# Kernel tuning notes

Measured on AMD Instinct MI355X. Metric: run time of the kernel, lower is better.

Reference implementation:

```python
import jax, jax.numpy as jnp
import numpy as np

N = 100_000      # nodes
E = 1_600_000    # edges (avg degree 16)
IN_DIM = 256
HID = 128
N_OUT = 2


def _linear_params(key, fan_in, fan_out):
    kw, kb = jax.random.split(key)
    bound = 1.0 / np.sqrt(fan_in)
    W = jax.random.uniform(kw, (fan_in, fan_out), jnp.float32, -bound, bound)
    b = jax.random.uniform(kb, (fan_out,), jnp.float32, -bound, bound)
    return W, b


def setup_inputs() -> dict:
    key = jax.random.key(0)
    ks = jax.random.split(key, 6)
    edge_index = jax.random.randint(ks[0], (2, E), 0, N, dtype=jnp.int64)
    x = jax.random.normal(ks[1], (N, IN_DIM), jnp.float32)
    Wi, bi = _linear_params(ks[2], IN_DIM, HID)   # NodeInitializer.lin
    W1, b1 = _linear_params(ks[3], HID, HID)      # GCNConv 1
    W2, b2 = _linear_params(ks[4], HID, HID)      # GCNConv 2
    Wh, bh = _linear_params(ks[5], HID, N_OUT)    # head
    return {"edge_index": edge_index, "x": x, "Wi": Wi, "bi": bi,
            "W1": W1, "b1": b1, "W2": W2, "b2": b2, "Wh": Wh, "bh": bh}


def reference(edge_index, x, Wi, bi, W1, b1, W2, b2, Wh, bh):
    n = x.shape[0]
    # GCNConv preprocessing: add self-loops, symmetric degree normalization.
    loops = jnp.arange(n, dtype=edge_index.dtype)
    src = jnp.concatenate([edge_index[0], loops])  # message source
    dst = jnp.concatenate([edge_index[1], loops])  # aggregation target
    deg = jax.ops.segment_sum(jnp.ones(src.shape[0], jnp.float32), dst, num_segments=n)
    dinv = jnp.where(deg > 0, deg ** -0.5, 0.0)
    norm = dinv[src] * dinv[dst]                   # [E+N]

    # NodeInitializer: relu(linear(x)); dropout = identity (eval mode)
    h = jax.nn.relu(x @ Wi + bi)

    # Two GCNConv layers (no relu between, matching SimpleGCN.forward)
    for W, b in ((W1, b1), (W2, b2)):
        msg = (h @ W)[src] * norm[:, None]         # gather + normalize, [E+N, HID]
        h = jax.ops.segment_sum(msg, dst, num_segments=n) + b  # scatter-add

    return h @ Wh + bh                             # [N, N_OUT]
```

## Files before the change

kernel.cpp:

```cpp
#include <hip/hip_runtime.h>
#include <hip/hip_bf16.h>

#define N_NODES 100000
#define N_EDGES 1600000
#define DIM_IN  256
#define DIM_H   128

#define NBKT 782
#define CPAD 16
#define EPB  8192
#define NBLK ((N_EDGES + EPB - 1) / EPB)

typedef __attribute__((ext_vector_type(8))) short short8;
typedef __attribute__((ext_vector_type(4))) float f32x4;

__device__ __forceinline__ int get_src(const int* e, int is64, int i) {
  return is64 ? e[2 * i] : e[i];
}
__device__ __forceinline__ int get_dst(const int* e, int is64, int i) {
  return is64 ? e[2 * (N_EDGES + i)] : e[N_EDGES + i];
}

__global__ __launch_bounds__(1024)
void k_init(const int* __restrict__ e, int* __restrict__ flag,
            int* __restrict__ bcnt) {
  if (blockIdx.x == 0) {
    __shared__ int s;
    if (threadIdx.x == 0) s = 0;
    __syncthreads();
    atomicOr(&s, e[2 * threadIdx.x + 1]);
    __syncthreads();
    if (threadIdx.x == 0) *flag = (s == 0) ? 1 : 0;
  } else {
    int i = (blockIdx.x - 1) * 1024 + threadIdx.x;
    if (i < NBKT * CPAD) bcnt[i] = 0;
  }
}

__global__ __launch_bounds__(256) void k_zero(int* __restrict__ p, int n) {
  int i = blockIdx.x * 256 + threadIdx.x;
  if (i < n) p[i] = 0;
}

__global__ __launch_bounds__(1024)
void k_binc(const int* __restrict__ eidx, const int* __restrict__ flag,
            int* __restrict__ bcnt) {
  __shared__ int hist[NBKT];
  const int t = threadIdx.x;
  const int is64 = *flag;
  for (int i = t; i < NBKT; i += 1024) hist[i] = 0;
  __syncthreads();
#pragma unroll
  for (int j = 0; j < EPB / 1024; ++j) {
    int e = blockIdx.x * EPB + j * 1024 + t;
    if (e < N_EDGES) {
      unsigned s = (unsigned)get_src(eidx, is64, e);
      unsigned d = (unsigned)get_dst(eidx, is64, e);
      if (s < N_NODES && d < N_NODES) atomicAdd(&hist[d >> 7], 1);
    }
  }
  __syncthreads();
  for (int i = t; i < NBKT; i += 1024) {
    int h = hist[i];
    if (h) atomicAdd(&bcnt[i * CPAD], h);
  }
}

__global__ __launch_bounds__(1024)
void k_bscan(int* __restrict__ bcnt, int* __restrict__ bbase) {
  __shared__ int sm[1024];
  int t = threadIdx.x;
  int v = (t < NBKT) ? bcnt[t * CPAD] : 0;
  sm[t] = v;
  __syncthreads();
  for (int d = 1; d < 1024; d <<= 1) {
    int u = (t >= d) ? sm[t - d] : 0;
    __syncthreads();
    sm[t] += u;
    __syncthreads();
  }
  if (t < NBKT) {
    int excl = sm[t] - v;
    bbase[t] = excl;
    bcnt[t * CPAD] = excl;
    if (t == NBKT - 1) bbase[NBKT] = sm[t];
  }
}

__global__ __launch_bounds__(1024)
void k_bin(const int* __restrict__ eidx, const int* __restrict__ flag,
           int* __restrict__ bcnt, unsigned* __restrict__ ebuf) {
  __shared__ int hist[NBKT];
  __shared__ int cur[NBKT];
  const int t = threadIdx.x;
  const int is64 = *flag;
  for (int i = t; i < NBKT; i += 1024) hist[i] = 0;
  unsigned rec[EPB / 1024];
  int bkt[EPB / 1024];
  __syncthreads();
#pragma unroll
  for (int j = 0; j < EPB / 1024; ++j) {
    int e = blockIdx.x * EPB + j * 1024 + t;
    bkt[j] = -1;
    rec[j] = 0;
    if (e < N_EDGES) {
      unsigned s = (unsigned)get_src(eidx, is64, e);
      unsigned d = (unsigned)get_dst(eidx, is64, e);
      if (s < N_NODES && d < N_NODES) {
        bkt[j] = (int)(d >> 7);
        rec[j] = s | ((d & 127u) << 17);
        atomicAdd(&hist[bkt[j]], 1);
      }
    }
  }
  __syncthreads();
  for (int i = t; i < NBKT; i += 1024) {
    int h = hist[i];
    cur[i] = h ? atomicAdd(&bcnt[i * CPAD], h) : 0;
  }
  __syncthreads();
#pragma unroll
  for (int j = 0; j < EPB / 1024; ++j) {
    if (bkt[j] >= 0) {
      int pos = atomicAdd(&cur[bkt[j]], 1);
      ebuf[pos] = rec[j];
    }
  }
}

__global__ __launch_bounds__(256)
void k_csr(const int* __restrict__ bbase, const unsigned* __restrict__ ebuf,
           int* __restrict__ off, float* __restrict__ dinv,
           int* __restrict__ csr) {
  __shared__ int hist[128];
  __shared__ int scn[128];
  __shared__ int cur[128];
  const int b = blockIdx.x, t = threadIdx.x;
  const int n0 = b << 7;
  const int start = bbase[b], end = bbase[b + 1];
  if (t < 128) hist[t] = 0;
  __syncthreads();
  for (int i = start + t; i < end; i += 256) {
    atomicAdd(&hist[ebuf[i] >> 17], 1);
  }
  __syncthreads();
  if (t < 128) scn[t] = hist[t];
  __syncthreads();
  for (int d = 1; d < 128; d <<= 1) {
    int u = (t < 128 && t >= d) ? scn[t - d] : 0;
    __syncthreads();
    if (t < 128) scn[t] += u;
    __syncthreads();
  }
  if (t < 128) {
    int node = n0 + t;
    if (node < N_NODES) {
      off[node] = start + scn[t];
      dinv[node] = rsqrtf(1.0f + (float)hist[t]);
      cur[t] = start + scn[t] - hist[t];
    }
  }
  __syncthreads();
  for (int i = start + t; i < end; i += 256) {
    unsigned r = ebuf[i];
    int pos = atomicAdd(&cur[r >> 17], 1);
    csr[pos] = (int)(r & 0x1FFFFu);
  }
}

__device__ __forceinline__ ushort f2bf(float f) {
  unsigned u = __float_as_uint(f);
  unsigned r = (u + 0x7fffu + ((u >> 16) & 1u)) >> 16;
  return (ushort)r;
}
__device__ __forceinline__ float bf2f(ushort h) {
  return __uint_as_float(((unsigned)h) << 16);
}

__device__ __forceinline__ void load8(const float* p, float* o) {
  float4 a = reinterpret_cast<const float4*>(p)[0];
  float4 b = reinterpret_cast<const float4*>(p)[1];
  o[0] = a.x; o[1] = a.y; o[2] = a.z; o[3] = a.w;
  o[4] = b.x; o[5] = b.y; o[6] = b.z; o[7] = b.w;
}

__device__ __forceinline__ void cvt_split(const float* v, short8& h, short8& l) {
#pragma unroll
  for (int j = 0; j < 8; ++j) {
    ushort hb = f2bf(v[j]);
    ushort lb = f2bf(v[j] - bf2f(hb));
    h[j] = (short)hb;
    l[j] = (short)lb;
  }
}

__global__ __launch_bounds__(256)
void k_prep(const float* __restrict__ Wi, const float* __restrict__ W1,
            const float* __restrict__ W2, const float* __restrict__ Wh,
            const float* __restrict__ b1, const float* __restrict__ b2,
            const float* __restrict__ bh, ushort* __restrict__ outHi,
            float* __restrict__ Wcc) {
  __shared__ float Wc2s[DIM_H][2];
  constexpr int CH = DIM_IN / 32;
  if (blockIdx.x == 16) {
    const int t = threadIdx.x;
    const int i = t >> 1, j = t & 1;
    float s = 0.f;
#pragma unroll 4
    for (int m = 0; m < DIM_H; ++m) s += W2[(size_t)i * DIM_H + m] * Wh[m * 2 + j];
    Wc2s[i][j] = s;
    __syncthreads();
    float c = 0.f;
#pragma unroll 4
    for (int k = 0; k < DIM_H; ++k) c += W1[(size_t)i * DIM_H + k] * Wc2s[k][j];
    Wcc[i * 2 + j] = c;
    if (t < 2) {
      float a = 0.f, b = 0.f;
      for (int k = 0; k < DIM_H; ++k) {
        a += b1[k] * Wc2s[k][t];
        b += b2[k] * Wh[k * 2 + t];
      }
      Wcc[256 + t] = a;
      Wcc[258 + t] = b + bh[t];
    }
    return;
  }
  int idx = blockIdx.x * 256 + threadIdx.x;
  int n  = idx & 15;
  int qq = (idx >> 4) & 3;
  int nt = (idx >> 6) & 7;
  int c  = idx >> 9;
  int col = nt * 16 + n;
  short8 h8, l8;
#pragma unroll
  for (int j = 0; j < 8; ++j) {
    float v = Wi[(size_t)(c * 32 + qq * 8 + j) * DIM_H + col];
    ushort hb = f2bf(v);
    ushort lb = f2bf(v - bf2f(hb));
    h8[j] = (short)hb;
    l8[j] = (short)lb;
  }
  ((short8*)outHi)[idx] = h8;
  ((short8*)outHi)[CH * 512 + idx] = l8;
}

template <int K>
__global__ __launch_bounds__(256, 4)
void k_gemm_xz(const float* __restrict__ A, const ushort* __restrict__ Bfrag,
               const float* __restrict__ bias, const float* __restrict__ Wcc,
               const float* __restrict__ dinv, float4* __restrict__ tbl) {
  constexpr int CH = K / 32;
  __shared__ __align__(16) ushort AhiS[2][256 * 8];
  __shared__ __align__(16) ushort AloS[2][256 * 8];
  const int tid = threadIdx.x;
  const int m0 = blockIdx.x * 64;
  const int wave = tid >> 6, lane = tid & 63;
  const int m_l = lane & 15, quad = lane >> 4;
  const int rs = tid >> 2, q = tid & 3;

  f32x4 acc[2][4];
#pragma unroll
  for (int i = 0; i < 2; ++i)
#pragma unroll
    for (int j = 0; j < 4; ++j) acc[i][j] = (f32x4){0.f, 0.f, 0.f, 0.f};

  const short8* Bhi8 = (const short8*)Bfrag;
  const short8* Blo8 = Bhi8 + CH * 512;
  short8* Ah = (short8*)AhiS;
  short8* Al = (short8*)AloS;

  const int gr = m0 + rs;
  const float* Ap = &A[(size_t)((gr < N_NODES) ? gr : (N_NODES - 1)) * K + q * 8];
  const int went = (rs >> 4) * 64 + q * 16 + ((rs & 15) ^ (q << 2));
  const int rent = quad * 16 + (m_l ^ (quad << 2));

  {
    float v[8];
    load8(Ap, v);
    short8 h, l;
    cvt_split(v, h, l);
    Ah[went] = h;
    Al[went] = l;
  }
  const int bq = quad * 16 + m_l;
  short8 bh0 = Bhi8[(wave * 2 + 0) * 64 + bq];
  short8 bl0 = Blo8[(wave * 2 + 0) * 64 + bq];
  short8 bh1 = Bhi8[(wave * 2 + 1) * 64 + bq];
  short8 bl1 = Blo8[(wave * 2 + 1) * 64 + bq];
  __syncthreads();

#pragma unroll
  for (int c = 0; c < CH; ++c) {
    const int cur = c & 1, nxt = cur ^ 1;
    float vn[8];
    short8 nbh0, nbl0, nbh1, nbl1;
    if (c + 1 < CH) {
      load8(Ap + (c + 1) * 32, vn);
      const int b0 = ((c + 1) * 8 + wave * 2 + 0) * 64 + bq;
      const int b1 = ((c + 1) * 8 + wave * 2 + 1) * 64 + bq;
      nbh0 = Bhi8[b0]; nbl0 = Blo8[b0];
      nbh1 = Bhi8[b1]; nbl1 = Blo8[b1];
    }
    const short8* AhC = Ah + cur * 256;
    const short8* AlC = Al + cur * 256;
#pragma unroll
    for (int mt = 0; mt < 4; ++mt) {
      short8 ahi = AhC[mt * 64 + rent];
      short8 alo = AlC[mt * 64 + rent];
      acc[0][mt] = __builtin_amdgcn_mfma_f32_16x16x32_bf16(ahi, bh0, acc[0][mt], 0, 0, 0);
      acc[0][mt] = __builtin_amdgcn_mfma_f32_16x16x32_bf16(ahi, bl0, acc[0][mt], 0, 0, 0);
      acc[0][mt] = __builtin_amdgcn_mfma_f32_16x16x32_bf16(alo, bh0, acc[0][mt], 0, 0, 0);
      acc[1][mt] = __builtin_amdgcn_mfma_f32_16x16x32_bf16(ahi, bh1, acc[1][mt], 0, 0, 0);
      acc[1][mt] = __builtin_amdgcn_mfma_f32_16x16x32_bf16(ahi, bl1, acc[1][mt], 0, 0, 0);
      acc[1][mt] = __builtin_amdgcn_mfma_f32_16x16x32_bf16(alo, bh1, acc[1][mt], 0, 0, 0);
    }
    if (c + 1 < CH) {
      short8 h, l;
      cvt_split(vn, h, l);
      Ah[nxt * 256 + went] = h;
      Al[nxt * 256 + went] = l;
      bh0 = nbh0; bl0 = nbl0; bh1 = nbh1; bl1 = nbl1;
    }
    __syncthreads();
  }

  float p0[4][4], p1[4][4];
#pragma unroll
  for (int mt = 0; mt < 4; ++mt)
#pragma unroll
    for (int r = 0; r < 4; ++r) { p0[mt][r] = 0.f; p1[mt][r] = 0.f; }
#pragma unroll
  for (int ntl = 0; ntl < 2; ++ntl) {
    const int colg = (wave * 2 + ntl) * 16 + m_l;
    const float bv = bias[colg];
    const float w0 = Wcc[colg * 2 + 0];
    const float w1 = Wcc[colg * 2 + 1];
#pragma unroll
    for (int mt = 0; mt < 4; ++mt)
#pragma unroll
      for (int r = 0; r < 4; ++r) {
        float hv = fmaxf(acc[ntl][mt][r] + bv, 0.f);
        p0[mt][r] += hv * w0;
        p1[mt][r] += hv * w1;
      }
  }
#pragma unroll
  for (int o = 1; o < 16; o <<= 1) {
#pragma unroll
    for (int mt = 0; mt < 4; ++mt)
#pragma unroll
      for (int r = 0; r < 4; ++r) {
        p0[mt][r] += __shfl_xor(p0[mt][r], o);
        p1[mt][r] += __shfl_xor(p1[mt][r], o);
      }
  }
  float* zred = (float*)AhiS;
  if (m_l == 0) {
#pragma unroll
    for (int mt = 0; mt < 4; ++mt)
#pragma unroll
      for (int r = 0; r < 4; ++r) {
        zred[(((0 * 4 + wave) * 4 + quad) * 4 + mt) * 4 + r] = p0[mt][r];
        zred[(((1 * 4 + wave) * 4 + quad) * 4 + mt) * 4 + r] = p1[mt][r];
      }
  }
  __syncthreads();
  if (tid < 64) {
    const int mt = tid >> 4, qd = (tid >> 2) & 3, r = tid & 3;
    const int rowg = m0 + tid;
    if (rowg < N_NODES) {
      float s0 = 0.f, s1 = 0.f;
#pragma unroll
      for (int w = 0; w < 4; ++w) {
        s0 += zred[(((0 * 4 + w) * 4 + qd) * 4 + mt) * 4 + r];
        s1 += zred[(((1 * 4 + w) * 4 + qd) * 4 + mt) * 4 + r];
      }
      float dn = dinv[rowg];
      tbl[rowg] = make_float4(dn * s0, dn * s1, dn, 0.f);
    }
  }
}

__global__ __launch_bounds__(256)
void k_aggr1(const int* __restrict__ off, const int* __restrict__ csr,
             const float4* __restrict__ tbl, float2* __restrict__ tb2,
             float* __restrict__ g) {
  int node = blockIdx.x * 256 + threadIdx.x;
  if (node >= N_NODES) return;
  int start = (node == 0) ? 0 : off[node - 1];
  int end = off[node];
  float4 self = tbl[node];
  float s0 = self.x, s1 = self.y, sd = self.z;
  int e = start;
  for (; e + 3 < end; e += 4) {
    int i0 = csr[e], i1 = csr[e + 1], i2 = csr[e + 2], i3 = csr[e + 3];
    float4 v0 = tbl[i0];
    float4 v1 = tbl[i1];
    float4 v2 = tbl[i2];
    float4 v3 = tbl[i3];
    s0 += (v0.x + v1.x) + (v2.x + v3.x);
    s1 += (v0.y + v1.y) + (v2.y + v3.y);
    sd += (v0.z + v1.z) + (v2.z + v3.z);
  }
  for (; e < end; ++e) {
    float4 v = tbl[csr[e]];
    s0 += v.x; s1 += v.y; sd += v.z;
  }
  float dn = self.z;
  tb2[node] = make_float2(dn * dn * s0, dn * dn * s1);
  g[node] = dn * sd;
}

__global__ __launch_bounds__(256)
void k_aggr2(const int* __restrict__ off, const int* __restrict__ csr,
             const float2* __restrict__ tb2, const float* __restrict__ dinv,
             const float* __restrict__ g, const float* __restrict__ tail,
             float* __restrict__ out) {
  int node = blockIdx.x * 256 + threadIdx.x;
  if (node >= N_NODES) return;
  int start = (node == 0) ? 0 : off[node - 1];
  int end = off[node];
  float2 self = tb2[node];
  float s0 = self.x, s1 = self.y;
  int e = start;
  for (; e + 3 < end; e += 4) {
    int i0 = csr[e], i1 = csr[e + 1], i2 = csr[e + 2], i3 = csr[e + 3];
    float2 v0 = tb2[i0];
    float2 v1 = tb2[i1];
    float2 v2 = tb2[i2];
    float2 v3 = tb2[i3];
    s0 += (v0.x + v1.x) + (v2.x + v3.x);
    s1 += (v0.y + v1.y) + (v2.y + v3.y);
  }
  for (; e < end; ++e) {
    float2 v = tb2[csr[e]];
    s0 += v.x; s1 += v.y;
  }
  float dn = dinv[node], gv = g[node];
  float o0 = dn * s0 + gv * tail[0] + tail[2];
  float o1 = dn * s1 + gv * tail[1] + tail[3];
  reinterpret_cast<float2*>(out)[node] = make_float2(o0, o1);
}

__global__ __launch_bounds__(256) void k_count(const int* __restrict__ eidx,
                                               const int* __restrict__ flag,
                                               int* __restrict__ off) {
  int e = blockIdx.x * 256 + threadIdx.x;
  int is64 = *flag;
  if (e < N_EDGES) {
    unsigned d = (unsigned)get_dst(eidx, is64, e);
    if (d < N_NODES) atomicAdd(&off[d], 1);
  }
}

__global__ __launch_bounds__(256) void k_dinv_old(const int* __restrict__ off,
                                                  float* __restrict__ dinv) {
  int i = blockIdx.x * 256 + threadIdx.x;
  if (i < N_NODES) dinv[i] = rsqrtf(1.0f + (float)off[i]);
}

template <int K>
__global__ __launch_bounds__(256)
void k_gemm(const float* __restrict__ A, const float* __restrict__ B,
            const float* __restrict__ bias, const float* __restrict__ scale,
            float* __restrict__ C, const int do_relu) {
  __shared__ float As[64][33];
  const int tid = threadIdx.x;
  const int tx = tid & 15;
  const int ty = tid >> 4;
  const int m0 = blockIdx.x * 64;

  float acc[4][8];
#pragma unroll
  for (int i = 0; i < 4; ++i)
#pragma unroll
    for (int j = 0; j < 8; ++j) acc[i][j] = 0.f;

  const int rs = tid >> 2;
  const int ks = (tid & 3) * 8;

  for (int k0 = 0; k0 < K; k0 += 32) {
    float av8[8];
    const int gm = m0 + rs;
    if (gm < N_NODES) {
      load8(&A[(size_t)gm * K + k0 + ks], av8);
    } else {
#pragma unroll
      for (int j = 0; j < 8; ++j) av8[j] = 0.f;
    }
    __syncthreads();
#pragma unroll
    for (int j = 0; j < 8; ++j) As[rs][ks + j] = av8[j];
    __syncthreads();

    const float* Bp = B + (size_t)k0 * DIM_H + tx * 8;
#pragma unroll 4
    for (int k = 0; k < 32; ++k) {
      float bv[8];
      load8(Bp + (size_t)k * DIM_H, bv);
      float av[4];
#pragma unroll
      for (int rr = 0; rr < 4; ++rr) av[rr] = As[ty * 4 + rr][k];
#pragma unroll
      for (int rr = 0; rr < 4; ++rr)
#pragma unroll
        for (int cc = 0; cc < 8; ++cc)
          acc[rr][cc] = fmaf(av[rr], bv[cc], acc[rr][cc]);
    }
  }

  float bs[8];
  if (bias) {
    load8(bias + tx * 8, bs);
  } else {
#pragma unroll
    for (int j = 0; j < 8; ++j) bs[j] = 0.f;
  }
#pragma unroll
  for (int rr = 0; rr < 4; ++rr) {
    const int gm = m0 + ty * 4 + rr;
    if (gm < N_NODES) {
      float sc = scale ? scale[gm] : 1.0f;
      float v[8];
#pragma unroll
      for (int cc = 0; cc < 8; ++cc) {
        float t = acc[rr][cc] + bs[cc];
        if (do_relu) t = fmaxf(t, 0.f);
        v[cc] = t * sc;
      }
      float* Cp = &C[(size_t)gm * DIM_H + tx * 8];
      reinterpret_cast<float4*>(Cp)[0] = make_float4(v[0], v[1], v[2], v[3]);
      reinterpret_cast<float4*>(Cp)[1] = make_float4(v[4], v[5], v[6], v[7]);
    }
  }
}

__global__ __launch_bounds__(256)
void k_aggr_init(const float* __restrict__ t, const float* __restrict__ dinv,
                 const float* __restrict__ bias, float* __restrict__ h) {
  int idx = blockIdx.x * 256 + threadIdx.x;
  if (idx < N_NODES * DIM_H) {
    int i = idx >> 7;
    int c = idx & 127;
    float d = dinv[i];
    h[idx] = bias[c] + t[idx] * d * d;
  }
}

__global__ __launch_bounds__(256)
void k_aggr_edges(const int* __restrict__ eidx, const int* __restrict__ flag,
                  const float* __restrict__ t, const float* __restrict__ dinv,
                  float* __restrict__ h) {
  int e = blockIdx.x * 2 + (threadIdx.x >> 7);
  int c = threadIdx.x & 127;
  int is64 = *flag;
  if (e < N_EDGES) {
    unsigned s = (unsigned)get_src(eidx, is64, e);
    unsigned d = (unsigned)get_dst(eidx, is64, e);
    if (s < N_NODES && d < N_NODES) {
      float nrm = dinv[s] * dinv[d];
      unsafeAtomicAdd(&h[(size_t)d * DIM_H + c], t[(size_t)s * DIM_H + c] * nrm);
    }
  }
}

__global__ __launch_bounds__(256)
void k_head_f32(const float* __restrict__ h, const float* __restrict__ Wh,
                const float* __restrict__ bh, float* __restrict__ out) {
  int node = blockIdx.x * 4 + (threadIdx.x >> 6);
  int lane = threadIdx.x & 63;
  if (node >= N_NODES) return;
  float h0 = h[(size_t)node * DIM_H + lane];
  float h1 = h[(size_t)node * DIM_H + 64 + lane];
  float s0 = h0 * Wh[lane * 2 + 0] + h1 * Wh[(lane + 64) * 2 + 0];
  float s1 = h0 * Wh[lane * 2 + 1] + h1 * Wh[(lane + 64) * 2 + 1];
#pragma unroll
  for (int off = 32; off > 0; off >>= 1) {
    s0 += __shfl_down(s0, off);
    s1 += __shfl_down(s1, off);
  }
  if (lane == 0) {
    reinterpret_cast<float2*>(out)[node] = make_float2(s0 + bh[0], s1 + bh[1]);
  }
}

extern "C" void kernel_launch(void* const* d_in, const int* in_sizes, int n_in,
                              void* d_out, int out_size, void* d_ws, size_t ws_size,
                              hipStream_t stream) {
  (void)in_sizes; (void)n_in; (void)out_size;
  const int* eidx = (const int*)d_in[0];
  const float* x  = (const float*)d_in[1];
  const float* Wi = (const float*)d_in[2];
  const float* bi = (const float*)d_in[3];
  const float* W1 = (const float*)d_in[4];
  const float* b1 = (const float*)d_in[5];
  const float* W2 = (const float*)d_in[6];
  const float* b2 = (const float*)d_in[7];
  const float* Wh = (const float*)d_in[8];
  const float* bh = (const float*)d_in[9];
  float* out = (float*)d_out;

  const int gE  = (N_EDGES + 255) / 256;
  const int gM  = (N_NODES + 63) / 64;
  const int gW  = (N_NODES + 3) / 4;
  const int gN256 = (N_NODES + 255) / 256;

  char* ws = (char*)d_ws;
  int* flag = (int*)ws;

  const size_t need1 = 17410048;

  if (ws_size >= need1) {
    int*      bcnt  = (int*)(ws + 4096);
    int*      bbase = (int*)(ws + 57344);
    float*    Wcc   = (float*)(ws + 61440);
    ushort*   bfWi  = (ushort*)(ws + 65536);
    int*      off   = (int*)(ws + 262144);
    float*    dinv  = (float*)(ws + 720896);
    float*    g     = (float*)(ws + 1179648);
    float4*   tbl   = (float4*)(ws + 1638400);
    float2*   tb2   = (float2*)(ws + 3407872);
    int*      csr   = (int*)(ws + 4456448);
    unsigned* ebuf  = (unsigned*)(ws + 11010048);

    k_init<<<1 + (NBKT * CPAD + 1023) / 1024, 1024, 0, stream>>>(eidx, flag, bcnt);
    k_binc<<<NBLK, 1024, 0, stream>>>(eidx, flag, bcnt);
    k_bscan<<<1, 1024, 0, stream>>>(bcnt, bbase);
    k_bin<<<NBLK, 1024, 0, stream>>>(eidx, flag, bcnt, ebuf);
    k_csr<<<NBKT, 256, 0, stream>>>(bbase, ebuf, off, dinv, csr);

    k_prep<<<17, 256, 0, stream>>>(Wi, W1, W2, Wh, b1, b2, bh, bfWi, Wcc);

    k_gemm_xz<DIM_IN><<<gM, 256, 0, stream>>>(x, bfWi, bi, Wcc, dinv, tbl);
    k_aggr1<<<gN256, 256, 0, stream>>>(off, csr, tbl, tb2, g);
    k_aggr2<<<gN256, 256, 0, stream>>>(off, csr, tb2, dinv, g, Wcc + 256, out);
  } else {
    const int gN  = (N_NODES + 255) / 256;
    int*   off  = (int*)(ws + 4096);
    float* dinv = (float*)(ws + 404480);
    float* fbA  = (float*)(ws + 804864);
    float* fbB  = (float*)(ws + 804864 + (size_t)N_NODES * DIM_H * 4);
    const int gNH = (N_NODES * DIM_H + 255) / 256;
    const int gE2 = (N_EDGES + 1) / 2;
    k_init<<<1, 1024, 0, stream>>>(eidx, flag, (int*)(ws + 4096));
    k_zero<<<gN, 256, 0, stream>>>(off, N_NODES);
    k_count<<<gE, 256, 0, stream>>>(eidx, flag, off);
    k_dinv_old<<<gN, 256, 0, stream>>>(off, dinv);

    k_gemm<DIM_IN><<<gM, 256, 0, stream>>>(x, Wi, bi, nullptr, fbA, 1);
    k_gemm<DIM_H><<<gM, 256, 0, stream>>>(fbA, W1, nullptr, nullptr, fbB, 0);
    k_aggr_init<<<gNH, 256, 0, stream>>>(fbB, dinv, b1, fbA);
    k_aggr_edges<<<gE2, 256, 0, stream>>>(eidx, flag, fbB, dinv, fbA);
    k_gemm<DIM_H><<<gM, 256, 0, stream>>>(fbA, W2, nullptr, nullptr, fbB, 0);
    k_aggr_init<<<gNH, 256, 0, stream>>>(fbB, dinv, b2, fbA);
    k_aggr_edges<<<gE2, 256, 0, stream>>>(eidx, flag, fbB, dinv, fbA);
    k_head_f32<<<gW, 256, 0, stream>>>(fbA, Wh, bh, out);
  }
}
```

Before: 285.3 us.

## Replace CSR build and gather aggregation with atomic edge scatter

Drops the multi-kernel bucket sort and CSR construction (binc, bscan, bin, csr). Degrees are now counted with global atomics and the two aggregations become per-edge scatter kernels with float atomics into zeroed accumulators, each followed by a per-node finalize kernel. This removes the sorting passes and their large edge buffers, at the cost of contended global float atomics in every layer and non-deterministic summation order. The fallback path now also uses k_init to zero its buffers instead of k_zero.

```diff
diff --git a/kernel.cpp b/kernel.cpp
--- a/kernel.cpp
+++ b/kernel.cpp
@@ -6,24 +6,13 @@
 #define DIM_IN  256
 #define DIM_H   128
 
-#define NBKT 782
-#define CPAD 16
-#define EPB  8192
-#define NBLK ((N_EDGES + EPB - 1) / EPB)
-
 typedef __attribute__((ext_vector_type(8))) short short8;
 typedef __attribute__((ext_vector_type(4))) float f32x4;
 
-__device__ __forceinline__ int get_src(const int* e, int is64, int i) {
-  return is64 ? e[2 * i] : e[i];
-}
-__device__ __forceinline__ int get_dst(const int* e, int is64, int i) {
-  return is64 ? e[2 * (N_EDGES + i)] : e[N_EDGES + i];
-}
-
 __global__ __launch_bounds__(1024)
 void k_init(const int* __restrict__ e, int* __restrict__ flag,
-            int* __restrict__ bcnt) {
+            int* __restrict__ deg, float* __restrict__ z1,
+            float* __restrict__ z2) {
   if (blockIdx.x == 0) {
     __shared__ int s;
     if (threadIdx.x == 0) s = 0;
@@ -33,139 +22,27 @@
     if (threadIdx.x == 0) *flag = (s == 0) ? 1 : 0;
   } else {
     int i = (blockIdx.x - 1) * 1024 + threadIdx.x;
-    if (i < NBKT * CPAD) bcnt[i] = 0;
-  }
-}
-
-__global__ __launch_bounds__(256) void k_zero(int* __restrict__ p, int n) {
+    if (i < N_NODES) deg[i] = 0;
+    if (i < 4 * N_NODES) z1[i] = 0.f;
+    if (i < 2 * N_NODES) z2[i] = 0.f;
+  }
+}
+
+__global__ __launch_bounds__(256)
+void k_degc(const int* __restrict__ eidx, const int* __restrict__ flag,
+            int* __restrict__ deg) {
   int i = blockIdx.x * 256 + threadIdx.x;
-  if (i < n) p[i] = 0;
-}
-
-__global__ __launch_bounds__(1024)
-void k_binc(const int* __restrict__ eidx, const int* __restrict__ flag,
-            int* __restrict__ bcnt) {
-  __shared__ int hist[NBKT];
-  const int t = threadIdx.x;
+  if (i >= N_EDGES) return;
   const int is64 = *flag;
-  for (int i = t; i < NBKT; i += 1024) hist[i] = 0;
-  __syncthreads();
-#pragma unroll
-  for (int j = 0; j < EPB / 1024; ++j) {
-    int e = blockIdx.x * EPB + j * 1024 + t;
-    if (e < N_EDGES) {
-      unsigned s = (unsigned)get_src(eidx, is64, e);
-      unsigned d = (unsigned)get_dst(eidx, is64, e);
-      if (s < N_NODES && d < N_NODES) atomicAdd(&hist[d >> 7], 1);
-    }
-  }
-  __syncthreads();
-  for (int i = t; i < NBKT; i += 1024) {
-    int h = hist[i];
-    if (h) atomicAdd(&bcnt[i * CPAD], h);
-  }
-}
-
-__global__ __launch_bounds__(1024)
-void k_bscan(int* __restrict__ bcnt, int* __restrict__ bbase) {
-  __shared__ int sm[1024];
-  int t = threadIdx.x;
-  int v = (t < NBKT) ? bcnt[t * CPAD] : 0;
-  sm[t] = v;
-  __syncthreads();
-  for (int d = 1; d < 1024; d <<= 1) {
-    int u = (t >= d) ? sm[t - d] : 0;
-    __syncthreads();
-    sm[t] += u;
-    __syncthreads();
-  }
-  if (t < NBKT) {
-    int excl = sm[t] - v;
-    bbase[t] = excl;
-    bcnt[t * CPAD] = excl;
-    if (t == NBKT - 1) bbase[NBKT] = sm[t];
-  }
-}
-
-__global__ __launch_bounds__(1024)
-void k_bin(const int* __restrict__ eidx, const int* __restrict__ flag,
-           int* __restrict__ bcnt, unsigned* __restrict__ ebuf) {
-  __shared__ int hist[NBKT];
-  __shared__ int cur[NBKT];
-  const int t = threadIdx.x;
-  const int is64 = *flag;
-  for (int i = t; i < NBKT; i += 1024) hist[i] = 0;
-  unsigned rec[EPB / 1024];
-  int bkt[EPB / 1024];
-  __syncthreads();
-#pragma unroll
-  for (int j = 0; j < EPB / 1024; ++j) {
-    int e = blockIdx.x * EPB + j * 1024 + t;
-    bkt[j] = -1;
-    rec[j] = 0;
-    if (e < N_EDGES) {
-      unsigned s = (unsigned)get_src(eidx, is64, e);
-      unsigned d = (unsigned)get_dst(eidx, is64, e);
-      if (s < N_NODES && d < N_NODES) {
-        bkt[j] = (int)(d >> 7);
-        rec[j] = s | ((d & 127u) << 17);
-        atomicAdd(&hist[bkt[j]], 1);
-      }
-    }
-  }
-  __syncthreads();
-  for (int i = t; i < NBKT; i += 1024) {
-    int h = hist[i];
-    cur[i] = h ? atomicAdd(&bcnt[i * CPAD], h) : 0;
-  }
-  __syncthreads();
-#pragma unroll
-  for (int j = 0; j < EPB / 1024; ++j) {
-    if (bkt[j] >= 0) {
-      int pos = atomicAdd(&cur[bkt[j]], 1);
-      ebuf[pos] = rec[j];
-    }
-  }
-}
-
-__global__ __launch_bounds__(256)
-void k_csr(const int* __restrict__ bbase, const unsigned* __restrict__ ebuf,
-           int* __restrict__ off, float* __restrict__ dinv,
-           int* __restrict__ csr) {
-  __shared__ int hist[128];
-  __shared__ int scn[128];
-  __shared__ int cur[128];
-  const int b = blockIdx.x, t = threadIdx.x;
-  const int n0 = b << 7;
-  const int start = bbase[b], end = bbase[b + 1];
-  if (t < 128) hist[t] = 0;
-  __syncthreads();
-  for (int i = start + t; i < end; i += 256) {
-    atomicAdd(&hist[ebuf[i] >> 17], 1);
-  }
-  __syncthreads();
-  if (t < 128) scn[t] = hist[t];
-  __syncthreads();
-  for (int d = 1; d < 128; d <<= 1) {
-    int u = (t < 128 && t >= d) ? scn[t - d] : 0;
-    __syncthreads();
-    if (t < 128) scn[t] += u;
-    __syncthreads();
-  }
-  if (t < 128) {
-    int node = n0 + t;
-    if (node < N_NODES) {
-      off[node] = start + scn[t];
-      dinv[node] = rsqrtf(1.0f + (float)hist[t]);
-      cur[t] = start + scn[t] - hist[t];
-    }
-  }
-  __syncthreads();
-  for (int i = start + t; i < end; i += 256) {
-    unsigned r = ebuf[i];
-    int pos = atomicAdd(&cur[r >> 17], 1);
-    csr[pos] = (int)(r & 0x1FFFFu);
-  }
+  unsigned s, d;
+  if (is64) {
+    s = (unsigned)((const int2*)eidx)[i].x;
+    d = (unsigned)((const int2*)eidx)[N_EDGES + i].x;
+  } else {
+    s = (unsigned)eidx[i];
+    d = (unsigned)eidx[N_EDGES + i];
+  }
+  if (s < N_NODES && d < N_NODES) atomicAdd(&deg[d], 1);
 }
 
 __device__ __forceinline__ ushort f2bf(float f) {
@@ -248,7 +125,7 @@
 __global__ __launch_bounds__(256, 4)
 void k_gemm_xz(const float* __restrict__ A, const ushort* __restrict__ Bfrag,
                const float* __restrict__ bias, const float* __restrict__ Wcc,
-               const float* __restrict__ dinv, float4* __restrict__ tbl) {
+               const int* __restrict__ deg, float4* __restrict__ tbl) {
   constexpr int CH = K / 32;
   __shared__ __align__(16) ushort AhiS[2][256 * 8];
   __shared__ __align__(16) ushort AloS[2][256 * 8];
@@ -375,71 +252,82 @@
         s0 += zred[(((0 * 4 + w) * 4 + qd) * 4 + mt) * 4 + r];
         s1 += zred[(((1 * 4 + w) * 4 + qd) * 4 + mt) * 4 + r];
       }
-      float dn = dinv[rowg];
+      float dn = rsqrtf(1.0f + (float)deg[rowg]);
       tbl[rowg] = make_float4(dn * s0, dn * s1, dn, 0.f);
     }
   }
 }
 
 __global__ __launch_bounds__(256)
-void k_aggr1(const int* __restrict__ off, const int* __restrict__ csr,
-             const float4* __restrict__ tbl, float2* __restrict__ tb2,
-             float* __restrict__ g) {
-  int node = blockIdx.x * 256 + threadIdx.x;
-  if (node >= N_NODES) return;
-  int start = (node == 0) ? 0 : off[node - 1];
-  int end = off[node];
-  float4 self = tbl[node];
-  float s0 = self.x, s1 = self.y, sd = self.z;
-  int e = start;
-  for (; e + 3 < end; e += 4) {
-    int i0 = csr[e], i1 = csr[e + 1], i2 = csr[e + 2], i3 = csr[e + 3];
-    float4 v0 = tbl[i0];
-    float4 v1 = tbl[i1];
-    float4 v2 = tbl[i2];
-    float4 v3 = tbl[i3];
-    s0 += (v0.x + v1.x) + (v2.x + v3.x);
-    s1 += (v0.y + v1.y) + (v2.y + v3.y);
-    sd += (v0.z + v1.z) + (v2.z + v3.z);
-  }
-  for (; e < end; ++e) {
-    float4 v = tbl[csr[e]];
-    s0 += v.x; s1 += v.y; sd += v.z;
-  }
-  float dn = self.z;
-  tb2[node] = make_float2(dn * dn * s0, dn * dn * s1);
-  g[node] = dn * sd;
-}
-
-__global__ __launch_bounds__(256)
-void k_aggr2(const int* __restrict__ off, const int* __restrict__ csr,
-             const float2* __restrict__ tb2, const float* __restrict__ dinv,
-             const float* __restrict__ g, const float* __restrict__ tail,
-             float* __restrict__ out) {
-  int node = blockIdx.x * 256 + threadIdx.x;
-  if (node >= N_NODES) return;
-  int start = (node == 0) ? 0 : off[node - 1];
-  int end = off[node];
-  float2 self = tb2[node];
-  float s0 = self.x, s1 = self.y;
-  int e = start;
-  for (; e + 3 < end; e += 4) {
-    int i0 = csr[e], i1 = csr[e + 1], i2 = csr[e + 2], i3 = csr[e + 3];
-    float2 v0 = tb2[i0];
-    float2 v1 = tb2[i1];
-    float2 v2 = tb2[i2];
-    float2 v3 = tb2[i3];
-    s0 += (v0.x + v1.x) + (v2.x + v3.x);
-    s1 += (v0.y + v1.y) + (v2.y + v3.y);
-  }
-  for (; e < end; ++e) {
-    float2 v = tb2[csr[e]];
-    s0 += v.x; s1 += v.y;
-  }
-  float dn = dinv[node], gv = g[node];
-  float o0 = dn * s0 + gv * tail[0] + tail[2];
-  float o1 = dn * s1 + gv * tail[1] + tail[3];
-  reinterpret_cast<float2*>(out)[node] = make_float2(o0, o1);
+void k_scat1(const int* __restrict__ eidx, const int* __restrict__ flag,
+             const float4* __restrict__ tbl, float4* __restrict__ acc1) {
+  int i = blockIdx.x * 256 + threadIdx.x;
+  if (i >= N_EDGES) return;
+  const int is64 = *flag;
+  unsigned s, d;
+  if (is64) {
+    s = (unsigned)((const int2*)eidx)[i].x;
+    d = (unsigned)((const int2*)eidx)[N_EDGES + i].x;
+  } else {
+    s = (unsigned)eidx[i];
+    d = (unsigned)eidx[N_EDGES + i];
+  }
+  if (s < N_NODES && d < N_NODES) {
+    float4 t = tbl[s];
+    float* a = (float*)(acc1 + d);
+    unsafeAtomicAdd(a + 0, t.x);
+    unsafeAtomicAdd(a + 1, t.y);
+    unsafeAtomicAdd(a + 2, t.z);
+  }
+}
+
+__global__ __launch_bounds__(256)
+void k_fin1(const float4* __restrict__ acc1, const float4* __restrict__ tbl,
+            float2* __restrict__ tb2, float* __restrict__ g) {
+  int n = blockIdx.x * 256 + threadIdx.x;
+  if (n >= N_NODES) return;
+  float4 a = acc1[n];
+  float4 t = tbl[n];
+  float dn = t.z;
+  tb2[n] = make_float2(dn * dn * (a.x + t.x), dn * dn * (a.y + t.y));
+  g[n] = dn * (a.z + t.z);
+}
+
+__global__ __launch_bounds__(256)
+void k_scat2(const int* __restrict__ eidx, const int* __restrict__ flag,
+             const float2* __restrict__ tb2, float2* __restrict__ acc2) {
+  int i = blockIdx.x * 256 + threadIdx.x;
+  if (i >= N_EDGES) return;
+  const int is64 = *flag;
+  unsigned s, d;
+  if (is64) {
+    s = (unsigned)((const int2*)eidx)[i].x;
+    d = (unsigned)((const int2*)eidx)[N_EDGES + i].x;
+  } else {
+    s = (unsigned)eidx[i];
+    d = (unsigned)eidx[N_EDGES + i];
+  }
+  if (s < N_NODES && d < N_NODES) {
+    float2 t = tb2[s];
+    float* a = (float*)(acc2 + d);
+    unsafeAtomicAdd(a + 0, t.x);
+    unsafeAtomicAdd(a + 1, t.y);
+  }
+}
+
+__global__ __launch_bounds__(256)
+void k_fin2(const float2* __restrict__ acc2, const float2* __restrict__ tb2,
+            const float4* __restrict__ tbl, const float* __restrict__ g,
+            const float* __restrict__ tail, float* __restrict__ out) {
+  int n = blockIdx.x * 256 + threadIdx.x;
+  if (n >= N_NODES) return;
+  float2 a = acc2[n];
+  float2 y = tb2[n];
+  float dn = tbl[n].z;
+  float gv = g[n];
+  float o0 = dn * (y.x + a.x) + gv * tail[0] + tail[2];
+  float o1 = dn * (y.y + a.y) + gv * tail[1] + tail[3];
+  reinterpret_cast<float2*>(out)[n] = make_float2(o0, o1);
 }
 
 __global__ __launch_bounds__(256) void k_count(const int* __restrict__ eidx,
@@ -448,7 +336,8 @@
   int e = blockIdx.x * 256 + threadIdx.x;
   int is64 = *flag;
   if (e < N_EDGES) {
-    unsigned d = (unsigned)get_dst(eidx, is64, e);
+    unsigned d = is64 ? (unsigned)((const int2*)eidx)[N_EDGES + e].x
+                      : (unsigned)eidx[N_EDGES + e];
     if (d < N_NODES) atomicAdd(&off[d], 1);
   }
 }
@@ -555,8 +444,9 @@
   int c = threadIdx.x & 127;
   int is64 = *flag;
   if (e < N_EDGES) {
-    unsigned s = (unsigned)get_src(eidx, is64, e);
-    unsigned d = (unsigned)get_dst(eidx, is64, e);
+    unsigned s = is64 ? (unsigned)((const int2*)eidx)[e].x : (unsigned)eidx[e];
+    unsigned d = is64 ? (unsigned)((const int2*)eidx)[N_EDGES + e].x
+                      : (unsigned)eidx[N_EDGES + e];
     if (s < N_NODES && d < N_NODES) {
       float nrm = dinv[s] * dinv[d];
       unsafeAtomicAdd(&h[(size_t)d * DIM_H + c], t[(size_t)s * DIM_H + c] * nrm);
@@ -604,48 +494,44 @@
   const int gM  = (N_NODES + 63) / 64;
   const int gW  = (N_NODES + 3) / 4;
   const int gN256 = (N_NODES + 255) / 256;
+  const int gZ  = 1 + (4 * N_NODES + 1023) / 1024;
 
   char* ws = (char*)d_ws;
   int* flag = (int*)ws;
 
-  const size_t need1 = 17410048;
+  const size_t need1 = 5739264;
 
   if (ws_size >= need1) {
-    int*      bcnt  = (int*)(ws + 4096);
-    int*      bbase = (int*)(ws + 57344);
-    float*    Wcc   = (float*)(ws + 61440);
-    ushort*   bfWi  = (ushort*)(ws + 65536);
-    int*      off   = (int*)(ws + 262144);
-    float*    dinv  = (float*)(ws + 720896);
-    float*    g     = (float*)(ws + 1179648);
-    float4*   tbl   = (float4*)(ws + 1638400);
-    float2*   tb2   = (float2*)(ws + 3407872);
-    int*      csr   = (int*)(ws + 4456448);
-    unsigned* ebuf  = (unsigned*)(ws + 11010048);
-
-    k_init<<<1 + (NBKT * CPAD + 1023) / 1024, 1024, 0, stream>>>(eidx, flag, bcnt);
-    k_binc<<<NBLK, 1024, 0, stream>>>(eidx, flag, bcnt);
-    k_bscan<<<1, 1024, 0, stream>>>(bcnt, bbase);
-    k_bin<<<NBLK, 1024, 0, stream>>>(eidx, flag, bcnt, ebuf);
-    k_csr<<<NBKT, 256, 0, stream>>>(bbase, ebuf, off, dinv, csr);
+    float*  Wcc  = (float*)(ws + 4096);
+    ushort* bfWi = (ushort*)(ws + 8192);
+    int*    deg  = (int*)(ws + 139264);
+    float4* tbl  = (float4*)(ws + 539264);
+    float4* acc1 = (float4*)(ws + 2139264);
+    float2* tb2  = (float2*)(ws + 3739264);
+    float*  g    = (float*)(ws + 4539264);
+    float2* acc2 = (float2*)(ws + 4939264);
+
+    k_init<<<gZ, 1024, 0, stream>>>(eidx, flag, deg, (float*)acc1, (float*)acc2);
+    k_degc<<<gE, 256, 0, stream>>>(eidx, flag, deg);
 
     k_prep<<<17, 256, 0, stream>>>(Wi, W1, W2, Wh, b1, b2, bh, bfWi, Wcc);
 
-    k_gemm_xz<DIM_IN><<<gM, 256, 0, stream>>>(x, bfWi, bi, Wcc, dinv, tbl);
-    k_aggr1<<<gN256, 256, 0, stream>>>(off, csr, tbl, tb2, g);
-    k_aggr2<<<gN256, 256, 0, stream>>>(off, csr, tb2, dinv, g, Wcc + 256, out);
+    k_gemm_xz<DIM_IN><<<gM, 256, 0, stream>>>(x, bfWi, bi, Wcc, deg, tbl);
+
+    k_scat1<<<gE, 256, 0, stream>>>(eidx, flag, tbl, acc1);
+    k_fin1<<<gN256, 256, 0, stream>>>(acc1, tbl, tb2, g);
+    k_scat2<<<gE, 256, 0, stream>>>(eidx, flag, tb2, acc2);
+    k_fin2<<<gN256, 256, 0, stream>>>(acc2, tb2, tbl, g, Wcc + 256, out);
   } else {
-    const int gN  = (N_NODES + 255) / 256;
     int*   off  = (int*)(ws + 4096);
     float* dinv = (float*)(ws + 404480);
     float* fbA  = (float*)(ws + 804864);
     float* fbB  = (float*)(ws + 804864 + (size_t)N_NODES * DIM_H * 4);
     const int gNH = (N_NODES * DIM_H + 255) / 256;
     const int gE2 = (N_EDGES + 1) / 2;
-    k_init<<<1, 1024, 0, stream>>>(eidx, flag, (int*)(ws + 4096));
-    k_zero<<<gN, 256, 0, stream>>>(off, N_NODES);
+    k_init<<<gZ, 1024, 0, stream>>>(eidx, flag, off, fbA, fbB);
     k_count<<<gE, 256, 0, stream>>>(eidx, flag, off);
-    k_dinv_old<<<gN, 256, 0, stream>>>(off, dinv);
+    k_dinv_old<<<gN256, 256, 0, stream>>>(off, dinv);
 
     k_gemm<DIM_IN><<<gM, 256, 0, stream>>>(x, Wi, bi, nullptr, fbA, 1);
     k_gemm<DIM_H><<<gM, 256, 0, stream>>>(fbA, W1, nullptr, nullptr, fbB, 0);
```

After: 689.5 us. 2.42x slower.

## Replace full CSR build with fixed-capacity bucket lists and shared-memory aggregation

Applied to the files above, without the earlier changes.

Drops the count, scan, bin and CSR kernels. Edges are now binned in one pass into per-bucket slots of fixed capacity (CAP=4096 per 128-node bucket). Degrees and both aggregation passes work per bucket with shared-memory float atomics, instead of per-node CSR walks. The int64 detection is folded into the binning kernel and the counter zeroing into the prep kernel. This removes several launches and a full edge reorder pass. The risks are overflow if a bucket gets more than CAP edges, nondeterministic float summation order, and shared atomic contention.

```diff
diff --git a/kernel.cpp b/kernel.cpp
--- a/kernel.cpp
+++ b/kernel.cpp
@@ -8,6 +8,7 @@
 
 #define NBKT 782
 #define CPAD 16
+#define CAP  4096
 #define EPB  8192
 #define NBLK ((N_EDGES + EPB - 1) / EPB)
 
@@ -19,153 +20,6 @@
 }
 __device__ __forceinline__ int get_dst(const int* e, int is64, int i) {
   return is64 ? e[2 * (N_EDGES + i)] : e[N_EDGES + i];
-}
-
-__global__ __launch_bounds__(1024)
-void k_init(const int* __restrict__ e, int* __restrict__ flag,
-            int* __restrict__ bcnt) {
-  if (blockIdx.x == 0) {
-    __shared__ int s;
-    if (threadIdx.x == 0) s = 0;
-    __syncthreads();
-    atomicOr(&s, e[2 * threadIdx.x + 1]);
-    __syncthreads();
-    if (threadIdx.x == 0) *flag = (s == 0) ? 1 : 0;
-  } else {
-    int i = (blockIdx.x - 1) * 1024 + threadIdx.x;
-    if (i < NBKT * CPAD) bcnt[i] = 0;
-  }
-}
-
-__global__ __launch_bounds__(256) void k_zero(int* __restrict__ p, int n) {
-  int i = blockIdx.x * 256 + threadIdx.x;
-  if (i < n) p[i] = 0;
-}
-
-__global__ __launch_bounds__(1024)
-void k_binc(const int* __restrict__ eidx, const int* __restrict__ flag,
-            int* __restrict__ bcnt) {
-  __shared__ int hist[NBKT];
-  const int t = threadIdx.x;
-  const int is64 = *flag;
-  for (int i = t; i < NBKT; i += 1024) hist[i] = 0;
-  __syncthreads();
-#pragma unroll
-  for (int j = 0; j < EPB / 1024; ++j) {
-    int e = blockIdx.x * EPB + j * 1024 + t;
-    if (e < N_EDGES) {
-      unsigned s = (unsigned)get_src(eidx, is64, e);
-      unsigned d = (unsigned)get_dst(eidx, is64, e);
-      if (s < N_NODES && d < N_NODES) atomicAdd(&hist[d >> 7], 1);
-    }
-  }
-  __syncthreads();
-  for (int i = t; i < NBKT; i += 1024) {
-    int h = hist[i];
-    if (h) atomicAdd(&bcnt[i * CPAD], h);
-  }
-}
-
-__global__ __launch_bounds__(1024)
-void k_bscan(int* __restrict__ bcnt, int* __restrict__ bbase) {
-  __shared__ int sm[1024];
-  int t = threadIdx.x;
-  int v = (t < NBKT) ? bcnt[t * CPAD] : 0;
-  sm[t] = v;
-  __syncthreads();
-  for (int d = 1; d < 1024; d <<= 1) {
-    int u = (t >= d) ? sm[t - d] : 0;
-    __syncthreads();
-    sm[t] += u;
-    __syncthreads();
-  }
-  if (t < NBKT) {
-    int excl = sm[t] - v;
-    bbase[t] = excl;
-    bcnt[t * CPAD] = excl;
-    if (t == NBKT - 1) bbase[NBKT] = sm[t];
-  }
-}
-
-__global__ __launch_bounds__(1024)
-void k_bin(const int* __restrict__ eidx, const int* __restrict__ flag,
-           int* __restrict__ bcnt, unsigned* __restrict__ ebuf) {
-  __shared__ int hist[NBKT];
-  __shared__ int cur[NBKT];
-  const int t = threadIdx.x;
-  const int is64 = *flag;
-  for (int i = t; i < NBKT; i += 1024) hist[i] = 0;
-  unsigned rec[EPB / 1024];
-  int bkt[EPB / 1024];
-  __syncthreads();
-#pragma unroll
-  for (int j = 0; j < EPB / 1024; ++j) {
-    int e = blockIdx.x * EPB + j * 1024 + t;
-    bkt[j] = -1;
-    rec[j] = 0;
-    if (e < N_EDGES) {
-      unsigned s = (unsigned)get_src(eidx, is64, e);
-      unsigned d = (unsigned)get_dst(eidx, is64, e);
-      if (s < N_NODES && d < N_NODES) {
-        bkt[j] = (int)(d >> 7);
-        rec[j] = s | ((d & 127u) << 17);
-        atomicAdd(&hist[bkt[j]], 1);
-      }
-    }
-  }
-  __syncthreads();
-  for (int i = t; i < NBKT; i += 1024) {
-    int h = hist[i];
-    cur[i] = h ? atomicAdd(&bcnt[i * CPAD], h) : 0;
-  }
-  __syncthreads();
-#pragma unroll
-  for (int j = 0; j < EPB / 1024; ++j) {
-    if (bkt[j] >= 0) {
-      int pos = atomicAdd(&cur[bkt[j]], 1);
-      ebuf[pos] = rec[j];
-    }
-  }
-}
-
-__global__ __launch_bounds__(256)
-void k_csr(const int* __restrict__ bbase, const unsigned* __restrict__ ebuf,
-           int* __restrict__ off, float* __restrict__ dinv,
-           int* __restrict__ csr) {
-  __shared__ int hist[128];
-  __shared__ int scn[128];
-  __shared__ int cur[128];
-  const int b = blockIdx.x, t = threadIdx.x;
-  const int n0 = b << 7;
-  const int start = bbase[b], end = bbase[b + 1];
-  if (t < 128) hist[t] = 0;
-  __syncthreads();
-  for (int i = start + t; i < end; i += 256) {
-    atomicAdd(&hist[ebuf[i] >> 17], 1);
-  }
-  __syncthreads();
-  if (t < 128) scn[t] = hist[t];
-  __syncthreads();
-  for (int d = 1; d < 128; d <<= 1) {
-    int u = (t < 128 && t >= d) ? scn[t - d] : 0;
-    __syncthreads();
-    if (t < 128) scn[t] += u;
-    __syncthreads();
-  }
-  if (t < 128) {
-    int node = n0 + t;
-    if (node < N_NODES) {
-      off[node] = start + scn[t];
-      dinv[node] = rsqrtf(1.0f + (float)hist[t]);
-      cur[t] = start + scn[t] - hist[t];
-    }
-  }
-  __syncthreads();
-  for (int i = start + t; i < end; i += 256) {
-    unsigned r = ebuf[i];
-    int pos = atomicAdd(&cur[r >> 17], 1);
-    csr[pos] = (int)(r & 0x1FFFFu);
-  }
 }
 
 __device__ __forceinline__ ushort f2bf(float f) {
@@ -199,9 +53,13 @@
             const float* __restrict__ W2, const float* __restrict__ Wh,
             const float* __restrict__ b1, const float* __restrict__ b2,
             const float* __restrict__ bh, ushort* __restrict__ outHi,
-            float* __restrict__ Wcc) {
+            float* __restrict__ Wcc, int* __restrict__ bcnt) {
   __shared__ float Wc2s[DIM_H][2];
   constexpr int CH = DIM_IN / 32;
+  if (blockIdx.x == 17) {
+    for (int i = threadIdx.x; i < NBKT * CPAD; i += 256) bcnt[i] = 0;
+    return;
+  }
   if (blockIdx.x == 16) {
     const int t = threadIdx.x;
     const int i = t >> 1, j = t & 1;
@@ -244,6 +102,69 @@
   ((short8*)outHi)[CH * 512 + idx] = l8;
 }
 
+__global__ __launch_bounds__(1024)
+void k_bin1(const int* __restrict__ eidx, int* __restrict__ bcnt,
+            unsigned* __restrict__ ebuf) {
+  __shared__ int hist[NBKT];
+  __shared__ int curL[NBKT];
+  __shared__ int s_or;
+  const int t = threadIdx.x;
+  if (t == 0) s_or = 0;
+  for (int i = t; i < NBKT; i += 1024) hist[i] = 0;
+  __syncthreads();
+  if (eidx[2 * t + 1] != 0) atomicOr(&s_or, 1);
+  __syncthreads();
+  const int is64 = (s_or == 0);
+
+  unsigned rec[EPB / 1024];
+  int bkt[EPB / 1024];
+#pragma unroll
+  for (int j = 0; j < EPB / 1024; ++j) {
+    int e = blockIdx.x * EPB + j * 1024 + t;
+    bkt[j] = -1;
+    rec[j] = 0;
+    if (e < N_EDGES) {
+      unsigned s = (unsigned)get_src(eidx, is64, e);
+      unsigned d = (unsigned)get_dst(eidx, is64, e);
+      if (s < N_NODES && d < N_NODES) {
+        bkt[j] = (int)(d >> 7);
+        rec[j] = s | ((d & 127u) << 17);
+        atomicAdd(&hist[bkt[j]], 1);
+      }
+    }
+  }
+  __syncthreads();
+  for (int i = t; i < NBKT; i += 1024) {
+    int h = hist[i];
+    curL[i] = h ? atomicAdd(&bcnt[i * CPAD], h) : 0;
+  }
+  __syncthreads();
+#pragma unroll
+  for (int j = 0; j < EPB / 1024; ++j) {
+    if (bkt[j] >= 0) {
+      int pos = atomicAdd(&curL[bkt[j]], 1);
+      ebuf[(size_t)bkt[j] * CAP + pos] = rec[j];
+    }
+  }
+}
+
+__global__ __launch_bounds__(256)
+void k_dinvB(const int* __restrict__ bcnt, const unsigned* __restrict__ ebuf,
+             float* __restrict__ dinv) {
+  __shared__ int hist[128];
+  const int b = blockIdx.x, t = threadIdx.x;
+  if (t < 128) hist[t] = 0;
+  __syncthreads();
+  const int cnt = bcnt[b * CPAD];
+  const unsigned* eb = ebuf + (size_t)b * CAP;
+  for (int i = t; i < cnt; i += 256) atomicAdd(&hist[eb[i] >> 17], 1);
+  __syncthreads();
+  if (t < 128) {
+    int node = (b << 7) + t;
+    if (node < N_NODES) dinv[node] = rsqrtf(1.0f + (float)hist[t]);
+  }
+}
+
 template <int K>
 __global__ __launch_bounds__(256, 4)
 void k_gemm_xz(const float* __restrict__ A, const ushort* __restrict__ Bfrag,
@@ -382,64 +303,81 @@
 }
 
 __global__ __launch_bounds__(256)
-void k_aggr1(const int* __restrict__ off, const int* __restrict__ csr,
-             const float4* __restrict__ tbl, float2* __restrict__ tb2,
-             float* __restrict__ g) {
-  int node = blockIdx.x * 256 + threadIdx.x;
-  if (node >= N_NODES) return;
-  int start = (node == 0) ? 0 : off[node - 1];
-  int end = off[node];
-  float4 self = tbl[node];
-  float s0 = self.x, s1 = self.y, sd = self.z;
-  int e = start;
-  for (; e + 3 < end; e += 4) {
-    int i0 = csr[e], i1 = csr[e + 1], i2 = csr[e + 2], i3 = csr[e + 3];
-    float4 v0 = tbl[i0];
-    float4 v1 = tbl[i1];
-    float4 v2 = tbl[i2];
-    float4 v3 = tbl[i3];
-    s0 += (v0.x + v1.x) + (v2.x + v3.x);
-    s1 += (v0.y + v1.y) + (v2.y + v3.y);
-    sd += (v0.z + v1.z) + (v2.z + v3.z);
-  }
-  for (; e < end; ++e) {
-    float4 v = tbl[csr[e]];
-    s0 += v.x; s1 += v.y; sd += v.z;
-  }
-  float dn = self.z;
-  tb2[node] = make_float2(dn * dn * s0, dn * dn * s1);
-  g[node] = dn * sd;
-}
-
-__global__ __launch_bounds__(256)
-void k_aggr2(const int* __restrict__ off, const int* __restrict__ csr,
-             const float2* __restrict__ tb2, const float* __restrict__ dinv,
-             const float* __restrict__ g, const float* __restrict__ tail,
-             float* __restrict__ out) {
-  int node = blockIdx.x * 256 + threadIdx.x;
-  if (node >= N_NODES) return;
-  int start = (node == 0) ? 0 : off[node - 1];
-  int end = off[node];
-  float2 self = tb2[node];
-  float s0 = self.x, s1 = self.y;
-  int e = start;
-  for (; e + 3 < end; e += 4) {
-    int i0 = csr[e], i1 = csr[e + 1], i2 = csr[e + 2], i3 = csr[e + 3];
-    float2 v0 = tb2[i0];
-    float2 v1 = tb2[i1];
-    float2 v2 = tb2[i2];
-    float2 v3 = tb2[i3];
-    s0 += (v0.x + v1.x) + (v2.x + v3.x);
-    s1 += (v0.y + v1.y) + (v2.y + v3.y);
-  }
-  for (; e < end; ++e) {
-    float2 v = tb2[csr[e]];
-    s0 += v.x; s1 += v.y;
-  }
-  float dn = dinv[node], gv = g[node];
-  float o0 = dn * s0 + gv * tail[0] + tail[2];
-  float o1 = dn * s1 + gv * tail[1] + tail[3];
-  reinterpret_cast<float2*>(out)[node] = make_float2(o0, o1);
+void k_aggr1B(const int* __restrict__ bcnt, const unsigned* __restrict__ ebuf,
+              const float4* __restrict__ tbl, float2* __restrict__ tb2,
+              float* __restrict__ g) {
+  __shared__ float acc[128][4];
+  const int b = blockIdx.x, t = threadIdx.x;
+  if (t < 128) { acc[t][0] = 0.f; acc[t][1] = 0.f; acc[t][2] = 0.f; }
+  __syncthreads();
+  const int cnt = bcnt[b * CPAD];
+  const unsigned* eb = ebuf + (size_t)b * CAP;
+  for (int i = t; i < cnt; i += 256) {
+    unsigned r = eb[i];
+    float4 v = tbl[r & 0x1FFFFu];
+    int d = r >> 17;
+    atomicAdd(&acc[d][0], v.x);
+    atomicAdd(&acc[d][1], v.y);
+    atomicAdd(&acc[d][2], v.z);
+  }
+  __syncthreads();
+  if (t < 128) {
+    int node = (b << 7) + t;
+    if (node < N_NODES) {
+      float4 self = tbl[node];
+      float dn = self.z;
+      tb2[node] = make_float2(dn * dn * (acc[t][0] + self.x),
+                              dn * dn * (acc[t][1] + self.y));
+      g[node] = dn * (acc[t][2] + self.z);
+    }
+  }
+}
+
+__global__ __launch_bounds__(256)
+void k_aggr2B(const int* __restrict__ bcnt, const unsigned* __restrict__ ebuf,
+              const float2* __restrict__ tb2, const float4* __restrict__ tbl,
+              const float* __restrict__ g, const float* __restrict__ tail,
+              float* __restrict__ out) {
+  __shared__ float acc[128][2];
+  const int b = blockIdx.x, t = threadIdx.x;
+  if (t < 128) { acc[t][0] = 0.f; acc[t][1] = 0.f; }
+  __syncthreads();
+  const int cnt = bcnt[b * CPAD];
+  const unsigned* eb = ebuf + (size_t)b * CAP;
+  for (int i = t; i < cnt; i += 256) {
+    unsigned r = eb[i];
+    float2 v = tb2[r & 0x1FFFFu];
+    int d = r >> 17;
+    atomicAdd(&acc[d][0], v.x);
+    atomicAdd(&acc[d][1], v.y);
+  }
+  __syncthreads();
+  if (t < 128) {
+    int node = (b << 7) + t;
+    if (node < N_NODES) {
+      float2 self = tb2[node];
+      float dn = tbl[node].z;
+      float gv = g[node];
+      float o0 = dn * (acc[t][0] + self.x) + gv * tail[0] + tail[2];
+      float o1 = dn * (acc[t][1] + self.y) + gv * tail[1] + tail[3];
+      reinterpret_cast<float2*>(out)[node] = make_float2(o0, o1);
+    }
+  }
+}
+
+__global__ __launch_bounds__(1024) void k_detect(const int* __restrict__ e,
+                                                 int* __restrict__ flag) {
+  __shared__ int s;
+  if (threadIdx.x == 0) s = 0;
+  __syncthreads();
+  atomicOr(&s, e[2 * threadIdx.x + 1]);
+  __syncthreads();
+  if (threadIdx.x == 0) *flag = (s == 0) ? 1 : 0;
+}
+
+__global__ __launch_bounds__(256) void k_zero(int* __restrict__ p, int n) {
+  int i = blockIdx.x * 256 + threadIdx.x;
+  if (i < n) p[i] = 0;
 }
 
 __global__ __launch_bounds__(256) void k_count(const int* __restrict__ eidx,
@@ -603,46 +541,37 @@
   const int gE  = (N_EDGES + 255) / 256;
   const int gM  = (N_NODES + 63) / 64;
   const int gW  = (N_NODES + 3) / 4;
-  const int gN256 = (N_NODES + 255) / 256;
 
   char* ws = (char*)d_ws;
-  int* flag = (int*)ws;
-
-  const size_t need1 = 17410048;
+
+  const size_t need1 = 16201600;
 
   if (ws_size >= need1) {
-    int*      bcnt  = (int*)(ws + 4096);
-    int*      bbase = (int*)(ws + 57344);
-    float*    Wcc   = (float*)(ws + 61440);
-    ushort*   bfWi  = (ushort*)(ws + 65536);
-    int*      off   = (int*)(ws + 262144);
-    float*    dinv  = (float*)(ws + 720896);
-    float*    g     = (float*)(ws + 1179648);
-    float4*   tbl   = (float4*)(ws + 1638400);
-    float2*   tb2   = (float2*)(ws + 3407872);
-    int*      csr   = (int*)(ws + 4456448);
-    unsigned* ebuf  = (unsigned*)(ws + 11010048);
-
-    k_init<<<1 + (NBKT * CPAD + 1023) / 1024, 1024, 0, stream>>>(eidx, flag, bcnt);
-    k_binc<<<NBLK, 1024, 0, stream>>>(eidx, flag, bcnt);
-    k_bscan<<<1, 1024, 0, stream>>>(bcnt, bbase);
-    k_bin<<<NBLK, 1024, 0, stream>>>(eidx, flag, bcnt, ebuf);
-    k_csr<<<NBKT, 256, 0, stream>>>(bbase, ebuf, off, dinv, csr);
-
-    k_prep<<<17, 256, 0, stream>>>(Wi, W1, W2, Wh, b1, b2, bh, bfWi, Wcc);
-
+    float*    Wcc  = (float*)(ws + 4096);
+    ushort*   bfWi = (ushort*)(ws + 8192);
+    int*      bcnt = (int*)(ws + 139264);
+    float*    dinv = (float*)(ws + 189312);
+    float4*   tbl  = (float4*)(ws + 589312);
+    float2*   tb2  = (float2*)(ws + 2189312);
+    float*    g    = (float*)(ws + 2989312);
+    unsigned* ebuf = (unsigned*)(ws + 3389312);
+
+    k_prep<<<18, 256, 0, stream>>>(Wi, W1, W2, Wh, b1, b2, bh, bfWi, Wcc, bcnt);
+    k_bin1<<<NBLK, 1024, 0, stream>>>(eidx, bcnt, ebuf);
+    k_dinvB<<<NBKT, 256, 0, stream>>>(bcnt, ebuf, dinv);
     k_gemm_xz<DIM_IN><<<gM, 256, 0, stream>>>(x, bfWi, bi, Wcc, dinv, tbl);
-    k_aggr1<<<gN256, 256, 0, stream>>>(off, csr, tbl, tb2, g);
-    k_aggr2<<<gN256, 256, 0, stream>>>(off, csr, tb2, dinv, g, Wcc + 256, out);
+    k_aggr1B<<<NBKT, 256, 0, stream>>>(bcnt, ebuf, tbl, tb2, g);
+    k_aggr2B<<<NBKT, 256, 0, stream>>>(bcnt, ebuf, tb2, tbl, g, Wcc + 256, out);
   } else {
     const int gN  = (N_NODES + 255) / 256;
+    int*   flag = (int*)ws;
     int*   off  = (int*)(ws + 4096);
     float* dinv = (float*)(ws + 404480);
     float* fbA  = (float*)(ws + 804864);
     float* fbB  = (float*)(ws + 804864 + (size_t)N_NODES * DIM_H * 4);
     const int gNH = (N_NODES * DIM_H + 255) / 256;
     const int gE2 = (N_EDGES + 1) / 2;
-    k_init<<<1, 1024, 0, stream>>>(eidx, flag, (int*)(ws + 4096));
+    k_detect<<<1, 1024, 0, stream>>>(eidx, flag);
     k_zero<<<gN, 256, 0, stream>>>(off, N_NODES);
     k_count<<<gE, 256, 0, stream>>>(eidx, flag, off);
     k_dinv_old<<<gN, 256, 0, stream>>>(off, dinv);
```

Result: slower. 291.2 us (+2.1%).
